# Performance work log

Measured on AMD Instinct MI355X. Metric: run time of the kernel, lower is better.

Reference implementation:

```python
import jax, jax.numpy as jnp
import numpy as np

ALPHA = 10.0
BETA = 2.0


def _l2norm(x):
    return x / jnp.linalg.norm(x, axis=1, keepdims=True)


def setup_inputs() -> dict:
    key = jax.random.key(0)
    k1, k2, k3 = jax.random.split(key, 3)
    n, C, d = 4096, 10000, 2048
    inputs = _l2norm(jax.random.normal(k1, (n, d), dtype=jnp.float32))
    kernel = _l2norm(jax.random.normal(k2, (C, d), dtype=jnp.float32))
    targets = jax.random.randint(k3, (n,), 0, C, dtype=jnp.int64 if jax.config.jax_enable_x64 else jnp.int32)
    return {"inputs": inputs, "targets": targets, "kernel": kernel}


def reference(inputs, targets, kernel):
    n = inputs.shape[0]
    C = kernel.shape[0]
    rows = jnp.arange(n)

    # cos_theta uses a detached kernel (no grad through this GEMM in original)
    cos = jnp.clip(inputs @ jax.lax.stop_gradient(kernel).T, -1.0, 1.0)  # [n, C]

    # phi_i = <inputs_i, kernel[targets_i]> - beta  (grad flows to kernel here)
    phi = jnp.sum(inputs * kernel[targets], axis=1) - BETA  # [n]

    pos_cos = cos[rows, targets]  # cos_theta at target columns, [n]
    mean_proxy_pos = pos_cos.sum() / n
    mean_proxy_neg = (cos.sum() - pos_cos.sum()) / (n * (C - 1))

    # output = cos_theta with target entries replaced by phi
    output = cos.at[rows, targets].set(phi)  # [n, C]
    onehot = jax.nn.one_hot(targets, C, dtype=output.dtype)

    loss_pos = phi  # sum(output * onehot, axis=1)
    loss_neg = jnp.log(jnp.sum(jnp.exp(output * ALPHA) * (1.0 - onehot), axis=1))  # [n]
    loss_mask = (jnp.max(output, axis=1) - phi) > 0.0
    per_sample = -loss_pos + loss_neg / ALPHA
    denom = jnp.maximum(loss_mask.sum(), 1).astype(per_sample.dtype)
    loss = jnp.sum(jnp.where(loss_mask, per_sample, 0.0)) / denom

    pred = jnp.argmax(output, axis=1)
    prec = jnp.mean((pred == targets).astype(jnp.float32))

    sim = inputs @ inputs.T  # [n, n]
    sim_label = (targets[:, None] == targets[None, :]).astype(sim.dtype)
    pos_cnt = sim_label.sum()
    neg_cnt = (n * n) - pos_cnt
    mean_pos_sim = jnp.sum(sim * sim_label) / pos_cnt
    mean_neg_sim = jnp.sum(sim * (1.0 - sim_label)) / neg_cnt

    return (loss, prec, mean_proxy_pos, mean_proxy_neg, mean_pos_sim, mean_neg_sim)
```

## Files before the change

kernel.cpp:

```cpp
#include <hip/hip_runtime.h>
#include <hip/hip_bf16.h>

#define NROWS 4096
#define NCLS  10000
#define DIM   2048
#define DIMB  1024
#define ALPHA_F 10.0f
#define BETA_F  2.0f
#define FP4_SCALE 64.0f
#define INVQ (1.0f / (FP4_SCALE * FP4_SCALE))

typedef float f32x4 __attribute__((ext_vector_type(4)));
typedef int   i32x4 __attribute__((ext_vector_type(4)));
typedef int   i32x8 __attribute__((ext_vector_type(8)));

__global__ void cast_fp4_kernel(const float* __restrict__ src,
                                unsigned int* __restrict__ dst, int n8) {
  int stride = gridDim.x * blockDim.x;
  for (int i = blockIdx.x * blockDim.x + threadIdx.x; i < n8; i += stride) {
    float4 a = reinterpret_cast<const float4*>(src)[2 * i];
    float4 b = reinterpret_cast<const float4*>(src)[2 * i + 1];
    float v[8] = {a.x, a.y, a.z, a.w, b.x, b.y, b.z, b.w};
    unsigned int w = 0;
#pragma unroll
    for (int j = 0; j < 8; ++j) {
      float s = v[j] * FP4_SCALE;
      float av = fabsf(s);
      unsigned int code = (unsigned)(av > 0.25f) + (av > 0.75f) + (av > 1.25f)
                        + (av > 1.75f) + (av > 2.5f) + (av > 3.5f) + (av > 5.0f);
      code |= (s < 0.f) ? 8u : 0u;
      w |= code << (4 * j);
    }
    dst[i] = w;
  }
}

__global__ void gather_dot_kernel(const float* __restrict__ X, const float* __restrict__ Kn,
                                  const int* __restrict__ tgt, float* __restrict__ dotv) {
  int gtid = blockIdx.x * blockDim.x + threadIdx.x;
  int wave = gtid >> 6;
  int lane = threadIdx.x & 63;
  if (wave >= NROWS) return;
  const float* xr = X + (size_t)wave * DIM;
  const float* kr = Kn + (size_t)tgt[wave] * DIM;
  float s = 0.f;
#pragma unroll
  for (int it = 0; it < DIM / 256; ++it) {
    int k = lane * 4 + it * 256;
    float4 a = *reinterpret_cast<const float4*>(xr + k);
    float4 b = *reinterpret_cast<const float4*>(kr + k);
    s += a.x * b.x + a.y * b.y + a.z * b.z + a.w * b.w;
  }
#pragma unroll
  for (int off = 32; off > 0; off >>= 1) s += __shfl_down(s, off);
  if (lane == 0) dotv[wave] = s;
}


#define STAGE_Q(MAT, BUF, SRC, RB, H, KT, NRW)                                  \
  { int lr = (H) * 64 + (tid >> 2);                                             \
    int gr = (RB) + lr; if (gr > (NRW) - 1) gr = (NRW) - 1;                     \
    const unsigned char* gp = (SRC) + (size_t)gr * DIMB + (KT) * 64             \
                               + ((sS ^ (lr & 3)) << 4);                        \
    unsigned char* lp = lds + (BUF) * 16384 + (MAT) * 8192 + lr * 64 + sS * 16; \
    __builtin_amdgcn_global_load_lds(                                           \
        (const __attribute__((address_space(1))) void*)gp,                      \
        (__attribute__((address_space(3))) void*)lp, 16, 0, 0); }

#define STAGE_TILE(BUF, KT)                                                     \
  STAGE_Q(0, BUF, A, rowBase, 0, KT, NROWS); STAGE_Q(0, BUF, A, rowBase, 1, KT, NROWS); \
  STAGE_Q(1, BUF, B, colBase, 0, KT, nBrows); STAGE_Q(1, BUF, B, colBase, 1, KT, nBrows);

#define RD_FRAG(dst, BUF, MAT, RC)                                              \
  { int r_ = (RC);                                                              \
    const unsigned char* p_ = lds + (BUF) * 16384 + (MAT) * 8192 + r_ * 64;     \
    i32x4 v_ = *reinterpret_cast<const i32x4*>(p_ + ((kg ^ (r_ & 3)) << 4));    \
    dst[0] = v_[0]; dst[1] = v_[1]; dst[2] = v_[2]; dst[3] = v_[3];             \
    dst[4] = 0; dst[5] = 0; dst[6] = 0; dst[7] = 0; }

template <int EP>
__global__ __launch_bounds__(256, 4)
void gemm_kernel(const unsigned char* __restrict__ A,
                 const unsigned char* __restrict__ B,
                 int nBrows,
                 const float* __restrict__ dotv,
                 const int* __restrict__ tgt,
                 float* __restrict__ S1, float* __restrict__ Eacc,
                 float* __restrict__ CNT, float* __restrict__ simAcc) {
  __shared__ unsigned char lds[2 * 16384];

  const int tid  = threadIdx.x;
  const int lane = tid & 63;
  const int wid  = tid >> 6;
  const int wr   = wid >> 1;
  const int wc   = wid & 1;
  const int fr   = lane & 15;
  const int kg   = lane >> 4;
  const int sS   = tid & 3;

  const int lin = blockIdx.x;
  int rowTile, colTile;
  if (EP == 0) {
    int swz = (lin & 7) * 320 + (lin >> 3);
    colTile = swz / 32;
    rowTile = swz % 32;
  } else {
    int swz = (lin & 7) * 66 + (lin >> 3);
    int r = 0;
    while ((r + 1) * (r + 2) / 2 <= swz) ++r;
    rowTile = r;
    colTile = swz - r * (r + 1) / 2;
  }
  const int rowBase = rowTile * 128;
  const int colBase = colTile * 128;

  f32x4 acc[4][4];
  const f32x4 zero = {0.f, 0.f, 0.f, 0.f};
#pragma unroll
  for (int m = 0; m < 4; ++m)
#pragma unroll
    for (int n = 0; n < 4; ++n) acc[m][n] = zero;

  STAGE_TILE(0, 0);
  __syncthreads();

#pragma unroll 1
  for (int kt = 0; kt < 16; ++kt) {
    const int buf = kt & 1;
    const int ktn = (kt < 15) ? kt + 1 : 15;
    STAGE_TILE(buf ^ 1, ktn);
    i32x8 afr[4], bfr[4];
#pragma unroll
    for (int m2 = 0; m2 < 4; ++m2)
      RD_FRAG(afr[m2], buf, 0, wr * 64 + m2 * 16 + fr);
#pragma unroll
    for (int n2 = 0; n2 < 4; ++n2)
      RD_FRAG(bfr[n2], buf, 1, wc * 64 + n2 * 16 + fr);
    __builtin_amdgcn_s_setprio(1);
#pragma unroll
    for (int m2 = 0; m2 < 4; ++m2)
#pragma unroll
      for (int n2 = 0; n2 < 4; ++n2)
        acc[m2][n2] = __builtin_amdgcn_mfma_scale_f32_16x16x128_f8f6f4(
            afr[m2], bfr[n2], acc[m2][n2], 4, 4, 0, 127, 0, 127);
    __builtin_amdgcn_s_setprio(0);
    __syncthreads();
  }

  __syncthreads();

  if (EP == 0) {
    float* shPhi = reinterpret_cast<float*>(lds);
    if (tid < 128) shPhi[tid] = dotv[rowBase + tid] - BETA_F;
    __syncthreads();
#pragma unroll
    for (int m = 0; m < 4; ++m) {
#pragma unroll
      for (int j = 0; j < 4; ++j) {
        int rl = wr * 64 + m * 16 + kg * 4 + j;
        float ph = shPhi[rl];
        float s1 = 0.f, ee = 0.f, ct = 0.f;
#pragma unroll
        for (int n = 0; n < 4; ++n) {
          int gcol = colBase + wc * 64 + n * 16 + fr;
          float c = acc[m][n][j] * INVQ;
          c = fminf(fmaxf(c, -1.f), 1.f);
          if (gcol < nBrows) {
            s1 += c;
            ee += __expf(ALPHA_F * c);
            ct += (c > ph) ? 1.f : 0.f;
          }
        }
#pragma unroll
        for (int o = 1; o < 16; o <<= 1) {
          s1 += __shfl_xor(s1, o);
          ee += __shfl_xor(ee, o);
          ct += __shfl_xor(ct, o);
        }
        if (fr == 0) {
          int grow = rowBase + rl;
          atomicAdd(&S1[grow], s1);
          atomicAdd(&Eacc[grow], ee);
          atomicAdd(&CNT[grow], ct);
        }
      }
    }
  } else {
    const float wgt = (rowTile == colTile) ? 1.f : 2.f;
    int* shT = reinterpret_cast<int*>(lds);
    float* redbuf = reinterpret_cast<float*>(lds + 4096);
    if (tid < 128) shT[tid] = tgt[rowBase + tid];
    else if (tid < 256) shT[tid] = tgt[colBase + (tid - 128)];
    __syncthreads();
    float ps = 0.f, als = 0.f, pc = 0.f;
#pragma unroll
    for (int m = 0; m < 4; ++m) {
#pragma unroll
      for (int j = 0; j < 4; ++j) {
        int rl = wr * 64 + m * 16 + kg * 4 + j;
        int tr = shT[rl];
#pragma unroll
        for (int n = 0; n < 4; ++n) {
          int cl = wc * 64 + n * 16 + fr;
          float c = acc[m][n][j] * INVQ;
          als += c;
          if (tr == shT[128 + cl]) { ps += c; pc += 1.f; }
        }
      }
    }
#pragma unroll
    for (int o = 1; o < 64; o <<= 1) {
      ps  += __shfl_xor(ps, o);
      als += __shfl_xor(als, o);
      pc  += __shfl_xor(pc, o);
    }
    if (lane == 0) {
      redbuf[wid * 3 + 0] = ps;
      redbuf[wid * 3 + 1] = als;
      redbuf[wid * 3 + 2] = pc;
    }
    __syncthreads();
    if (tid == 0) {
      float p = 0.f, a = 0.f, c2 = 0.f;
      for (int w = 0; w < 4; ++w) {
        p += redbuf[w * 3 + 0];
        a += redbuf[w * 3 + 1];
        c2 += redbuf[w * 3 + 2];
      }
      atomicAdd(&simAcc[0], wgt * p);
      atomicAdd(&simAcc[1], wgt * a);
      atomicAdd(&simAcc[2], wgt * c2);
    }
  }
}

__global__ void finalize_kernel(const float* __restrict__ dotv, const float* __restrict__ S1,
                                const float* __restrict__ Eacc, const float* __restrict__ CNT,
                                const float* __restrict__ simAcc, float* __restrict__ out) {
  __shared__ float sh[5][256];
  int tid = threadIdx.x;
  float sum_posc = 0.f, sum_s1 = 0.f, loss_sum = 0.f, mask_cnt = 0.f, correct = 0.f;
  for (int i = tid; i < NROWS; i += 256) {
    float d = dotv[i];
    float posc = fminf(fmaxf(d, -1.f), 1.f);
    float phi = d - BETA_F;
    sum_posc += posc;
    sum_s1 += S1[i];
    float e = Eacc[i] - __expf(ALPHA_F * posc);
    float cexcl = CNT[i] - 1.f;
    float per = -phi + __logf(e) / ALPHA_F;
    if (cexcl > 0.5f) { loss_sum += per; mask_cnt += 1.f; }
    else correct += 1.f;
  }
  sh[0][tid] = sum_posc; sh[1][tid] = sum_s1; sh[2][tid] = loss_sum;
  sh[3][tid] = mask_cnt; sh[4][tid] = correct;
  __syncthreads();
  for (int s = 128; s > 0; s >>= 1) {
    if (tid < s)
      for (int q = 0; q < 5; ++q) sh[q][tid] += sh[q][tid + s];
    __syncthreads();
  }
  if (tid == 0) {
    float posS = sh[0][0], s1S = sh[1][0], lossS = sh[2][0], maskS = sh[3][0], corr = sh[4][0];
    out[0] = lossS / fmaxf(maskS, 1.f);
    out[1] = corr / (float)NROWS;
    out[2] = posS / (float)NROWS;
    out[3] = (s1S - posS) / ((float)NROWS * (float)(NCLS - 1));
    float pos = simAcc[0], all = simAcc[1], pcnt = simAcc[2];
    out[4] = pos / pcnt;
    out[5] = (all - pos) / ((float)NROWS * (float)NROWS - pcnt);
  }
}

extern "C" void kernel_launch(void* const* d_in, const int* in_sizes, int n_in,
                              void* d_out, int out_size, void* d_ws, size_t ws_size,
                              hipStream_t stream) {
  const float* X  = (const float*)d_in[0];
  const int*   tg = (const int*)d_in[1];
  const float* Kn = (const float*)d_in[2];
  float* out = (float*)d_out;

  char* w = (char*)d_ws;
  unsigned char* f4A = (unsigned char*)w;
  unsigned char* f4B = f4A + (size_t)NROWS * DIMB;
  float* dotv   = (float*)(w + (size_t)NROWS * DIMB + (size_t)NCLS * DIMB);
  float* S1     = dotv + NROWS;
  float* Eacc   = S1 + NROWS;
  float* CNT    = Eacc + NROWS;
  float* simAcc = CNT + NROWS;

  hipMemsetAsync(S1, 0, (3 * NROWS + 4) * sizeof(float), stream);

  cast_fp4_kernel<<<2048, 256, 0, stream>>>(X, (unsigned int*)f4A, NROWS * DIM / 8);
  cast_fp4_kernel<<<2048, 256, 0, stream>>>(Kn, (unsigned int*)f4B, NCLS * DIM / 8);
  gather_dot_kernel<<<NROWS / 4, 256, 0, stream>>>(X, Kn, tg, dotv);

  gemm_kernel<0><<<2560, 256, 0, stream>>>(
      f4A, f4B, NCLS, dotv, nullptr, S1, Eacc, CNT, nullptr);
  gemm_kernel<1><<<528, 256, 0, stream>>>(
      f4A, f4A, NROWS, nullptr, tg, nullptr, nullptr, nullptr, simAcc);

  finalize_kernel<<<1, 256, 0, stream>>>(dotv, S1, Eacc, CNT, simAcc, out);
}
```

Baseline: 165.6 us.

## Merge GEMM launches and cast kernels, repack LDS staging with 8-way swizzle

The two cast kernels become one launch covering both matrices. The classifier GEMM and the similarity GEMM run as a single kernel, with each block picking its job from its block index, so the tail of the first GEMM can overlap with the second. LDS staging now packs two rows per 128-byte line with an 8-way XOR swizzle and precomputed global and LDS offsets, and launch bounds ask for 5 blocks per CU. The risks are extra branching and register pressure in the fused kernel, and a mix of epilogue types running in one grid.

New measurement: 307.3 us. 1.86x slower.

```diff
diff --git a/kernel.cpp b/kernel.cpp
--- a/kernel.cpp
+++ b/kernel.cpp
@@ -9,29 +9,34 @@
 #define BETA_F  2.0f
 #define FP4_SCALE 64.0f
 #define INVQ (1.0f / (FP4_SCALE * FP4_SCALE))
+#define NMAIN_BLK 2560
+#define NSIM_BLK  528
 
 typedef float f32x4 __attribute__((ext_vector_type(4)));
 typedef int   i32x4 __attribute__((ext_vector_type(4)));
 typedef int   i32x8 __attribute__((ext_vector_type(8)));
 
-__global__ void cast_fp4_kernel(const float* __restrict__ src,
-                                unsigned int* __restrict__ dst, int n8) {
+__global__ void cast_fp4_kernel(const float* __restrict__ X, const float* __restrict__ Kn,
+                                unsigned int* __restrict__ dA, unsigned int* __restrict__ dB,
+                                int nA8, int nT8) {
   int stride = gridDim.x * blockDim.x;
-  for (int i = blockIdx.x * blockDim.x + threadIdx.x; i < n8; i += stride) {
-    float4 a = reinterpret_cast<const float4*>(src)[2 * i];
-    float4 b = reinterpret_cast<const float4*>(src)[2 * i + 1];
+  for (int i = blockIdx.x * blockDim.x + threadIdx.x; i < nT8; i += stride) {
+    const float* src; unsigned int* dst; int j;
+    if (i < nA8) { src = X; dst = dA; j = i; } else { src = Kn; dst = dB; j = i - nA8; }
+    float4 a = reinterpret_cast<const float4*>(src)[2 * j];
+    float4 b = reinterpret_cast<const float4*>(src)[2 * j + 1];
     float v[8] = {a.x, a.y, a.z, a.w, b.x, b.y, b.z, b.w};
     unsigned int w = 0;
 #pragma unroll
-    for (int j = 0; j < 8; ++j) {
-      float s = v[j] * FP4_SCALE;
+    for (int q = 0; q < 8; ++q) {
+      float s = v[q] * FP4_SCALE;
       float av = fabsf(s);
       unsigned int code = (unsigned)(av > 0.25f) + (av > 0.75f) + (av > 1.25f)
                         + (av > 1.75f) + (av > 2.5f) + (av > 3.5f) + (av > 5.0f);
       code |= (s < 0.f) ? 8u : 0u;
-      w |= code << (4 * j);
-    }
-    dst[i] = w;
+      w |= code << (4 * q);
+    }
+    dst[j] = w;
   }
 }
 
@@ -57,32 +62,12 @@
 }
 
 
-#define STAGE_Q(MAT, BUF, SRC, RB, H, KT, NRW)                                  \
-  { int lr = (H) * 64 + (tid >> 2);                                             \
-    int gr = (RB) + lr; if (gr > (NRW) - 1) gr = (NRW) - 1;                     \
-    const unsigned char* gp = (SRC) + (size_t)gr * DIMB + (KT) * 64             \
-                               + ((sS ^ (lr & 3)) << 4);                        \
-    unsigned char* lp = lds + (BUF) * 16384 + (MAT) * 8192 + lr * 64 + sS * 16; \
-    __builtin_amdgcn_global_load_lds(                                           \
-        (const __attribute__((address_space(1))) void*)gp,                      \
-        (__attribute__((address_space(3))) void*)lp, 16, 0, 0); }
-
-#define STAGE_TILE(BUF, KT)                                                     \
-  STAGE_Q(0, BUF, A, rowBase, 0, KT, NROWS); STAGE_Q(0, BUF, A, rowBase, 1, KT, NROWS); \
-  STAGE_Q(1, BUF, B, colBase, 0, KT, nBrows); STAGE_Q(1, BUF, B, colBase, 1, KT, nBrows);
-
-#define RD_FRAG(dst, BUF, MAT, RC)                                              \
-  { int r_ = (RC);                                                              \
-    const unsigned char* p_ = lds + (BUF) * 16384 + (MAT) * 8192 + r_ * 64;     \
-    i32x4 v_ = *reinterpret_cast<const i32x4*>(p_ + ((kg ^ (r_ & 3)) << 4));    \
-    dst[0] = v_[0]; dst[1] = v_[1]; dst[2] = v_[2]; dst[3] = v_[3];             \
-    dst[4] = 0; dst[5] = 0; dst[6] = 0; dst[7] = 0; }
-
-template <int EP>
-__global__ __launch_bounds__(256, 4)
+#define AS1 const __attribute__((address_space(1))) void*
+#define AS3 __attribute__((address_space(3))) void*
+
+__global__ __launch_bounds__(256, 5)
 void gemm_kernel(const unsigned char* __restrict__ A,
-                 const unsigned char* __restrict__ B,
-                 int nBrows,
+                 const unsigned char* __restrict__ Bm,
                  const float* __restrict__ dotv,
                  const int* __restrict__ tgt,
                  float* __restrict__ S1, float* __restrict__ Eacc,
@@ -96,23 +81,63 @@
   const int wc   = wid & 1;
   const int fr   = lane & 15;
   const int kg   = lane >> 4;
-  const int sS   = tid & 3;
 
   const int lin = blockIdx.x;
-  int rowTile, colTile;
-  if (EP == 0) {
+  const bool isMain = lin < NMAIN_BLK;
+  int rowTile, colTile, nB;
+  const unsigned char* B;
+  if (isMain) {
     int swz = (lin & 7) * 320 + (lin >> 3);
     colTile = swz / 32;
     rowTile = swz % 32;
+    B = Bm; nB = NCLS;
   } else {
-    int swz = (lin & 7) * 66 + (lin >> 3);
+    int l2 = lin - NMAIN_BLK;
+    int swz = (l2 & 7) * 66 + (l2 >> 3);
     int r = 0;
     while ((r + 1) * (r + 2) / 2 <= swz) ++r;
     rowTile = r;
     colTile = swz - r * (r + 1) / 2;
+    B = A; nB = NROWS;
   }
   const int rowBase = rowTile * 128;
   const int colBase = colTile * 128;
+
+  const int l0  = tid >> 3;
+  const int sp  = tid & 7;
+  const int lg8 = sp ^ (l0 & 7);
+  const int shi = lg8 >> 2, sc16 = lg8 & 3;
+  const int rA0 = rowBase + 2 * l0 + shi;
+  const int rA1 = rA0 + 64;
+  int cB0 = colBase + 2 * l0 + shi;      if (cB0 > nB - 1) cB0 = nB - 1;
+  int cB1 = colBase + 64 + 2 * l0 + shi; if (cB1 > nB - 1) cB1 = nB - 1;
+  const unsigned char* pA0 = A + (size_t)rA0 * DIMB + sc16 * 16;
+  const unsigned char* pA1 = A + (size_t)rA1 * DIMB + sc16 * 16;
+  const unsigned char* pB0 = B + (size_t)cB0 * DIMB + sc16 * 16;
+  const unsigned char* pB1 = B + (size_t)cB1 * DIMB + sc16 * 16;
+  const int dOff = l0 * 128 + sp * 16;
+
+#define STAGE_TILE(BUF, KT)                                                     \
+  { int ko_ = (KT) * 64;                                                        \
+    unsigned char* d_ = lds + (BUF) * 16384 + dOff;                             \
+    __builtin_amdgcn_global_load_lds((AS1)(pA0 + ko_), (AS3)(d_),          16, 0, 0); \
+    __builtin_amdgcn_global_load_lds((AS1)(pA1 + ko_), (AS3)(d_ + 4096),   16, 0, 0); \
+    __builtin_amdgcn_global_load_lds((AS1)(pB0 + ko_), (AS3)(d_ + 8192),   16, 0, 0); \
+    __builtin_amdgcn_global_load_lds((AS1)(pB1 + ko_), (AS3)(d_ + 12288),  16, 0, 0); }
+
+  int offA[4], offB[4];
+#pragma unroll
+  for (int m2 = 0; m2 < 4; ++m2) {
+    int lr = wr * 64 + m2 * 16 + fr;
+    int l = lr >> 1;
+    offA[m2] = l * 128 + ((((lr & 1) * 4 + kg) ^ (l & 7)) << 4);
+  }
+#pragma unroll
+  for (int n2 = 0; n2 < 4; ++n2) {
+    int lc = wc * 64 + n2 * 16 + fr;
+    int l = lc >> 1;
+    offB[n2] = 8192 + l * 128 + ((((lc & 1) * 4 + kg) ^ (l & 7)) << 4);
+  }
 
   f32x4 acc[4][4];
   const f32x4 zero = {0.f, 0.f, 0.f, 0.f};
@@ -129,13 +154,20 @@
     const int buf = kt & 1;
     const int ktn = (kt < 15) ? kt + 1 : 15;
     STAGE_TILE(buf ^ 1, ktn);
+    const unsigned char* lb = lds + buf * 16384;
     i32x8 afr[4], bfr[4];
 #pragma unroll
-    for (int m2 = 0; m2 < 4; ++m2)
-      RD_FRAG(afr[m2], buf, 0, wr * 64 + m2 * 16 + fr);
-#pragma unroll
-    for (int n2 = 0; n2 < 4; ++n2)
-      RD_FRAG(bfr[n2], buf, 1, wc * 64 + n2 * 16 + fr);
+    for (int m2 = 0; m2 < 4; ++m2) {
+      i32x4 v_ = *reinterpret_cast<const i32x4*>(lb + offA[m2]);
+      afr[m2][0] = v_[0]; afr[m2][1] = v_[1]; afr[m2][2] = v_[2]; afr[m2][3] = v_[3];
+      afr[m2][4] = 0; afr[m2][5] = 0; afr[m2][6] = 0; afr[m2][7] = 0;
+    }
+#pragma unroll
+    for (int n2 = 0; n2 < 4; ++n2) {
+      i32x4 v_ = *reinterpret_cast<const i32x4*>(lb + offB[n2]);
+      bfr[n2][0] = v_[0]; bfr[n2][1] = v_[1]; bfr[n2][2] = v_[2]; bfr[n2][3] = v_[3];
+      bfr[n2][4] = 0; bfr[n2][5] = 0; bfr[n2][6] = 0; bfr[n2][7] = 0;
+    }
     __builtin_amdgcn_s_setprio(1);
 #pragma unroll
     for (int m2 = 0; m2 < 4; ++m2)
@@ -149,7 +181,7 @@
 
   __syncthreads();
 
-  if (EP == 0) {
+  if (isMain) {
     float* shPhi = reinterpret_cast<float*>(lds);
     if (tid < 128) shPhi[tid] = dotv[rowBase + tid] - BETA_F;
     __syncthreads();
@@ -165,7 +197,7 @@
           int gcol = colBase + wc * 64 + n * 16 + fr;
           float c = acc[m][n][j] * INVQ;
           c = fminf(fmaxf(c, -1.f), 1.f);
-          if (gcol < nBrows) {
+          if (gcol < NCLS) {
             s1 += c;
             ee += __expf(ALPHA_F * c);
             ct += (c > ph) ? 1.f : 0.f;
@@ -291,14 +323,13 @@
 
   hipMemsetAsync(S1, 0, (3 * NROWS + 4) * sizeof(float), stream);
 
-  cast_fp4_kernel<<<2048, 256, 0, stream>>>(X, (unsigned int*)f4A, NROWS * DIM / 8);
-  cast_fp4_kernel<<<2048, 256, 0, stream>>>(Kn, (unsigned int*)f4B, NCLS * DIM / 8);
+  const int nA8 = NROWS * DIM / 8, nT8 = nA8 + NCLS * DIM / 8;
+  cast_fp4_kernel<<<2048, 256, 0, stream>>>(X, Kn, (unsigned int*)f4A,
+                                            (unsigned int*)f4B, nA8, nT8);
   gather_dot_kernel<<<NROWS / 4, 256, 0, stream>>>(X, Kn, tg, dotv);
 
-  gemm_kernel<0><<<2560, 256, 0, stream>>>(
-      f4A, f4B, NCLS, dotv, nullptr, S1, Eacc, CNT, nullptr);
-  gemm_kernel<1><<<528, 256, 0, stream>>>(
-      f4A, f4A, NROWS, nullptr, tg, nullptr, nullptr, nullptr, simAcc);
+  gemm_kernel<<<NMAIN_BLK + NSIM_BLK, 256, 0, stream>>>(
+      f4A, f4B, dotv, tg, S1, Eacc, CNT, simAcc);
 
   finalize_kernel<<<1, 256, 0, stream>>>(dotv, S1, Eacc, CNT, simAcc, out);
 }
```
